# Performance work log

Measured on AMD Instinct MI355X. Metric: run time of the kernel, lower is better.

Reference implementation:

```python
import jax, jax.numpy as jnp
import numpy as np

DIM, N_HEAD, N_KV, HEAD_DIM = 4096, 32, 8, 128
B, S = 2, 2048


def apply_rotary_emb(x, freqs_cis):
    # x: [B, S, H, D]; freqs_cis: [S, D//2, 2]
    xs = x.reshape(x.shape[:-1] + (-1, 2))            # [B,S,H,D/2,2]
    f = freqs_cis.reshape(1, xs.shape[1], 1, xs.shape[3], 2)
    x0, x1 = xs[..., 0], xs[..., 1]
    f0, f1 = f[..., 0], f[..., 1]
    out = jnp.stack([x0 * f0 - x1 * f1, x0 * f1 + x1 * f0], axis=-1)
    return out.reshape(x.shape).astype(x.dtype)


def setup_inputs() -> dict:
    key = jax.random.key(0)
    k1, k2, k3, k4 = jax.random.split(key, 4)
    x = jax.random.normal(k1, (B, S, DIM), dtype=jnp.float32)
    freqs_cis = jax.random.normal(k2, (S, HEAD_DIM // 2, 2), dtype=jnp.float32)
    # causal boolean mask (True = attend)
    mask_cache = jnp.tril(jnp.ones((S, S), dtype=bool))[None, None]
    input_pos = jnp.arange(S, dtype=jnp.int32)
    total_head_dim = (N_HEAD + 2 * N_KV) * HEAD_DIM
    wqkv = jax.random.normal(k3, (total_head_dim, DIM), dtype=jnp.float32) * (DIM ** -0.5)
    wo = jax.random.normal(k4, (DIM, DIM), dtype=jnp.float32) * (DIM ** -0.5)
    return {"x": x, "freqs_cis": freqs_cis, "mask_cache": mask_cache,
            "input_pos": input_pos, "wqkv": wqkv, "wo": wo}


def reference(x, freqs_cis, mask_cache, input_pos, wqkv, wo):
    bsz, seqlen, _ = x.shape
    kv_size = N_KV * HEAD_DIM
    qkv = jnp.einsum('bsd,fd->bsf', x, wqkv)
    q, k, v = jnp.split(qkv, [DIM, DIM + kv_size], axis=-1)
    q = q.reshape(bsz, seqlen, N_HEAD, HEAD_DIM)
    k = k.reshape(bsz, seqlen, N_KV, HEAD_DIM)
    v = v.reshape(bsz, seqlen, N_KV, HEAD_DIM)
    q = apply_rotary_emb(q, freqs_cis)
    k = apply_rotary_emb(k, freqs_cis)
    q = q.transpose(0, 2, 1, 3)   # [B,Hq,S,D]
    k = k.transpose(0, 2, 1, 3)   # [B,Hkv,S,D]
    v = v.transpose(0, 2, 1, 3)
    # GQA: repeat kv heads to match query heads
    g = N_HEAD // N_KV
    k = jnp.repeat(k, g, axis=1)
    v = jnp.repeat(v, g, axis=1)
    scale = 1.0 / jnp.sqrt(jnp.asarray(HEAD_DIM, dtype=q.dtype))
    scores = jnp.einsum('bhqd,bhkd->bhqk', q, k) * scale
    neg_inf = jnp.asarray(jnp.finfo(scores.dtype).min, dtype=scores.dtype)
    scores = jnp.where(mask_cache, scores, neg_inf)
    attn = jax.nn.softmax(scores, axis=-1)
    y = jnp.einsum('bhqk,bhkd->bhqd', attn, v)
    y = y.transpose(0, 2, 1, 3).reshape(bsz, seqlen, DIM)
    return jnp.einsum('bsd,od->bso', y, wo)
```

## Files before the change

### kernel.cpp

```cpp
#include <hip/hip_runtime.h>
#include <hip/hip_bf16.h>

#define DIM   4096
#define NHEAD 32
#define NKV   8
#define HD    128
#define BATCH 2
#define SEQ   2048
#define M1    (BATCH*SEQ)
#define NF    ((NHEAD+2*NKV)*HD)

typedef __attribute__((ext_vector_type(8))) short short8;
typedef __attribute__((ext_vector_type(4))) short short4v;
typedef __attribute__((ext_vector_type(4))) float f32x4;

__device__ __forceinline__ float bf2f(short s) {
    unsigned u = ((unsigned)(unsigned short)s) << 16;
    return __builtin_bit_cast(float, u);
}
__device__ __forceinline__ short f2bf(float f) {
    unsigned u = __builtin_bit_cast(unsigned, f);
    u = u + 0x7fffu + ((u >> 16) & 1u);
    return (short)(u >> 16);
}

__device__ __forceinline__ void gload_lds16(const void* g, void* l) {
    __builtin_amdgcn_global_load_lds(
        (const __attribute__((address_space(1))) void*)g,
        (__attribute__((address_space(3))) void*)l, 16, 0, 0);
}

__global__ void f2bf_k(const float* __restrict__ src, short* __restrict__ dst, int n4) {
    int i = blockIdx.x * blockDim.x + threadIdx.x;
    if (i >= n4) return;
    float4 v = ((const float4*)src)[i];
    short4v o;
    o[0] = f2bf(v.x); o[1] = f2bf(v.y); o[2] = f2bf(v.z); o[3] = f2bf(v.w);
    ((short4v*)dst)[i] = o;
}

template<int OUT_BF16>
__global__ __launch_bounds__(512, 2) void gemm256(const short* __restrict__ A,
                                                  const short* __restrict__ Bm,
                                                  void* __restrict__ Cout,
                                                  int M, int N, int K) {
    __shared__ __align__(16) short As[2][2][128*64];
    __shared__ __align__(16) short Bs[2][2][128*64];
    const int nbn = N >> 8;
    const int nwg = gridDim.x;
    const int cpx = nwg >> 3;
    const int swz = (blockIdx.x & 7) * cpx + (blockIdx.x >> 3);
    const int brow = swz / nbn, bcol = swz % nbn;
    const int t = threadIdx.x, lane = t & 63, w = t >> 6;
    const int wm = w >> 2, wn = w & 3;
    const int l16 = lane & 15, lhi = lane >> 4, l7 = l16 & 7;
    const size_t abase = (size_t)brow * 256 * K;
    const size_t bbase = (size_t)bcol * 256 * K;
    const int sr = t >> 3;
    const int sc = t & 7;
    const int scl = sc ^ (sr & 7);
    f32x4 acc[8][4] = {};

    auto stageA = [&](int kt, int qm) {
#pragma unroll
        for (int i = 0; i < 2; ++i)
            gload_lds16(A + abase + (size_t)(i*128 + qm*64 + sr) * K + kt*64 + scl*8,
                        &As[kt & 1][qm][(i*64 + sr)*64 + sc*8]);
    };
    auto stageB = [&](int kt, int qn) {
#pragma unroll
        for (int i = 0; i < 2; ++i)
            gload_lds16(Bm + bbase + (size_t)((i*2 + (sr>>5))*64 + qn*32 + (sr & 31)) * K + kt*64 + scl*8,
                        &Bs[kt & 1][qn][(i*64 + sr)*64 + sc*8]);
    };

    const int NT = K >> 6;
    stageA(0, 0); stageB(0, 0); stageA(0, 1); stageB(0, 1);
    stageA(1, 0); stageB(1, 0);
    asm volatile("s_waitcnt vmcnt(4)" ::: "memory");
    __builtin_amdgcn_s_barrier();

    short8 a0[4][2], a1[4][2], b0[2][2], b1[2][2];

#define LD_A(dst, P, QM)                                                        \
    _Pragma("unroll") for (int mi = 0; mi < 4; ++mi)                            \
    _Pragma("unroll") for (int kk = 0; kk < 2; ++kk)                            \
        dst[mi][kk] = *(const short8*)&As[P][QM][(wm*64 + mi*16 + l16)*64 + (((kk*4 + lhi) ^ l7) * 8)];
#define LD_B(dst, P, QN)                                                        \
    _Pragma("unroll") for (int ni = 0; ni < 2; ++ni)                            \
    _Pragma("unroll") for (int kk = 0; kk < 2; ++kk)                            \
        dst[ni][kk] = *(const short8*)&Bs[P][QN][(wn*32 + ni*16 + l16)*64 + (((kk*4 + lhi) ^ l7) * 8)];
#define MMA(QM, QN, af, bf)                                                     \
    __builtin_amdgcn_s_barrier();                                               \
    __builtin_amdgcn_s_setprio(1);                                              \
    _Pragma("unroll") for (int kk = 0; kk < 2; ++kk)                            \
    _Pragma("unroll") for (int mi = 0; mi < 4; ++mi)                            \
    _Pragma("unroll") for (int ni = 0; ni < 2; ++ni)                            \
        acc[QM*4 + mi][QN*2 + ni] = __builtin_amdgcn_mfma_f32_16x16x32_bf16(    \
            af[mi][kk], bf[ni][kk], acc[QM*4 + mi][QN*2 + ni], 0, 0, 0);        \
    __builtin_amdgcn_s_setprio(0);                                              \
    __builtin_amdgcn_s_barrier();

    LD_A(a0, 0, 0)
    LD_B(b0, 0, 0)

    for (int cur = 0; cur < NT; ++cur) {
        const int d = cur & 1, dn = d ^ 1;
        LD_B(b1, d, 1)
        if (cur + 1 < NT) stageA(cur + 1, 1);
        MMA(0, 0, a0, b0)
        asm volatile("s_waitcnt vmcnt(2)" ::: "memory");
        LD_A(a1, d, 1)
        if (cur + 1 < NT) stageB(cur + 1, 1);
        MMA(0, 1, a0, b1)
        LD_A(a0, dn, 0)
        if (cur + 2 < NT) stageA(cur + 2, 0);
        MMA(1, 0, a1, b0)
        asm volatile("s_waitcnt vmcnt(2)" ::: "memory");
        LD_B(b0, dn, 0)
        if (cur + 2 < NT) stageB(cur + 2, 0);
        MMA(1, 1, a1, b1)
    }
#undef LD_A
#undef LD_B
#undef MMA

#pragma unroll
    for (int fm = 0; fm < 8; ++fm)
#pragma unroll
        for (int fn = 0; fn < 4; ++fn)
#pragma unroll
            for (int r = 0; r < 4; ++r) {
                size_t row = (size_t)brow*256 + wm*128 + fm*16 + lhi*4 + r;
                size_t col = (size_t)bcol*256 + wn*64 + fn*16 + l16;
                if (OUT_BF16)
                    ((short*)Cout)[row * N + col] = f2bf(acc[fm][fn][r]);
                else
                    ((float*)Cout)[row * N + col] = acc[fm][fn][r];
            }
}

__global__ void rope_split_k(const short* __restrict__ qkv,
                             const float* __restrict__ freqs,
                             short* __restrict__ qb, short* __restrict__ kb,
                             short* __restrict__ vg) {
    int tid  = blockIdx.x * blockDim.x + threadIdx.x;
    int colg = tid % (NF / 8);
    int row  = tid / (NF / 8);
    if (row >= M1) return;
    int b = row >> 11, s = row & 2047;
    int f = colg << 3;
    int h = f >> 7, d = f & 127;
    short8 v = *(const short8*)&qkv[(size_t)row * NF + f];
    if (h < NHEAD + NKV) {
        const float4 fa = *(const float4*)&freqs[(size_t)(s*64 + (d>>1)) * 2];
        const float4 fb = *(const float4*)&freqs[(size_t)(s*64 + (d>>1)) * 2 + 4];
        float fr[8] = {fa.x, fa.y, fa.z, fa.w, fb.x, fb.y, fb.z, fb.w};
        short8 o;
#pragma unroll
        for (int p = 0; p < 4; ++p) {
            float x0 = bf2f(v[2*p]), x1 = bf2f(v[2*p+1]);
            float c = fr[2*p], sn = fr[2*p+1];
            o[2*p]   = f2bf(x0 * c  - x1 * sn);
            o[2*p+1] = f2bf(x0 * sn + x1 * c);
        }
        if (h < NHEAD)
            *(short8*)&qb[((((size_t)b*NHEAD + h)*SEQ + s) << 7) + d] = o;
        else
            *(short8*)&kb[((((size_t)b*NKV + (h - NHEAD))*SEQ + s) << 7) + d] = o;
    } else {
        int kvh = h - NHEAD - NKV;
        size_t base = (((size_t)b*NKV + kvh) << 18) + (size_t)(s >> 5)*4096 + (s & 31);
#pragma unroll
        for (int j = 0; j < 8; ++j)
            vg[base + (size_t)(d + j) * 32] = v[j];
    }
}

__global__ __launch_bounds__(256, 3) void attn_k(const short* __restrict__ qb_,
                                                 const short* __restrict__ kb_,
                                                 const short* __restrict__ vg_,
                                                 short* __restrict__ yb) {
    __shared__ __align__(16) short Ks[2][32*128];
    __shared__ __align__(16) short Vs[2][128*32];
    __shared__ __align__(16) short Pw[4][32*40];
    const int bid = blockIdx.x;
    const int qt = 15 - (bid >> 6);
    const int bh = bid & 63;
    const int b = bh >> 5, h = bh & 31, kv = h >> 2;
    const int t = threadIdx.x, lane = t & 63, w = t >> 6;
    const int l16 = lane & 15, lhi = lane >> 4;
    const short* Qp = qb_ + (((size_t)(b*NHEAD + h)*SEQ + qt*128 + w*32) << 7);
    const short* Kp = kb_ + (((size_t)(b*NKV + kv)*SEQ) << 7);
    const short* Vp = vg_ + (((size_t)(b*NKV + kv)*SEQ) << 7);
    short8 qf[2][4];
#pragma unroll
    for (int qq = 0; qq < 2; ++qq)
#pragma unroll
        for (int kk = 0; kk < 4; ++kk)
            qf[qq][kk] = *(const short8*)&Qp[(qq*16 + l16)*HD + kk*32 + lhi*8];
    f32x4 oacc[2][8] = {};
    float mrow[2] = {-1e30f, -1e30f};
    float lsum[2] = {0.f, 0.f};
    const int NT = (qt + 1) * 4;
    const int qmaxw = qt*128 + w*32 + 31;
    const float sc = 0.08838834764831845f;

    auto stage = [&](int kt, int buf) {
#pragma unroll
        for (int i = 0; i < 2; ++i) {
            int L = i*256 + t;
            int r = L >> 4, s = L & 15;
            int gs = (s & 8) | ((s & 7) ^ (r & 7));
            gload_lds16(Kp + (size_t)kt*4096 + r*128 + gs*8, &Ks[buf][L*8]);
        }
#pragma unroll
        for (int i = 0; i < 2; ++i) {
            int L = i*256 + t;
            int r8 = L >> 3, s3 = L & 7;
            int gs = s3 ^ (r8 & 7);
            gload_lds16(Vp + (size_t)kt*4096 + (r8*8 + gs)*8, &Vs[buf][L*8]);
        }
    };

    stage(0, 0);
    __syncthreads();
    int cur = 0;
    for (int kt = 0; kt < NT; ++kt) {
        if (kt + 1 < NT) stage(kt + 1, cur ^ 1);
        if (kt*32 <= qmaxw) {
            f32x4 sT[2][2] = {};
#pragma unroll
            for (int kk = 0; kk < 4; ++kk) {
                short8 kf[2];
#pragma unroll
                for (int kb2 = 0; kb2 < 2; ++kb2) {
                    int row = kb2*16 + l16;
                    int ch  = kk*4 + lhi;
                    int chs = (ch & 8) | ((ch & 7) ^ (row & 7));
                    kf[kb2] = *(const short8*)&Ks[cur][row*128 + chs*8];
                }
#pragma unroll
                for (int kb2 = 0; kb2 < 2; ++kb2)
#pragma unroll
                    for (int qq = 0; qq < 2; ++qq)
                        sT[kb2][qq] = __builtin_amdgcn_mfma_f32_16x16x32_bf16(kf[kb2], qf[qq][kk], sT[kb2][qq], 0, 0, 0);
            }
#pragma unroll
            for (int qq = 0; qq < 2; ++qq) {
                int qg = qt*128 + w*32 + qq*16 + l16;
                float tmax = -1e30f;
#pragma unroll
                for (int kb2 = 0; kb2 < 2; ++kb2)
#pragma unroll
                    for (int r = 0; r < 4; ++r) {
                        int kg = kt*32 + kb2*16 + lhi*4 + r;
                        float sv = sT[kb2][qq][r] * sc;
                        sv = (kg > qg) ? -1e30f : sv;
                        sT[kb2][qq][r] = sv;
                        tmax = fmaxf(tmax, sv);
                    }
                tmax = fmaxf(tmax, __shfl_xor(tmax, 16, 64));
                tmax = fmaxf(tmax, __shfl_xor(tmax, 32, 64));
                float mn = fmaxf(mrow[qq], tmax);
                float alpha = __expf(mrow[qq] - mn);
                mrow[qq] = mn;
                float rsum = 0.f;
#pragma unroll
                for (int kb2 = 0; kb2 < 2; ++kb2) {
                    short4v pk;
#pragma unroll
                    for (int r = 0; r < 4; ++r) {
                        float p = __expf(sT[kb2][qq][r] - mn);
                        rsum += p;
                        pk[r] = f2bf(p);
                    }
                    *(short4v*)&Pw[w][(qq*16 + l16)*40 + kb2*16 + lhi*4] = pk;
                }
                rsum += __shfl_xor(rsum, 16, 64);
                rsum += __shfl_xor(rsum, 32, 64);
                lsum[qq] = lsum[qq]*alpha + rsum;
                float a4[4];
#pragma unroll
                for (int r = 0; r < 4; ++r)
                    a4[r] = __shfl(alpha, (lane & 48) | (lhi*4 + r), 64);
#pragma unroll
                for (int n = 0; n < 8; ++n)
#pragma unroll
                    for (int r = 0; r < 4; ++r)
                        oacc[qq][n][r] *= a4[r];
            }
            short8 pf[2];
#pragma unroll
            for (int qq = 0; qq < 2; ++qq)
                pf[qq] = *(const short8*)&Pw[w][(qq*16 + l16)*40 + lhi*8];
#pragma unroll
            for (int n = 0; n < 8; ++n) {
                int d   = n*16 + l16;
                int lch = d*4 + lhi;
                int phys = (lch & ~7) | ((lch & 7) ^ ((lch >> 3) & 7));
                short8 vf = *(const short8*)&Vs[cur][phys*8];
#pragma unroll
                for (int qq = 0; qq < 2; ++qq)
                    oacc[qq][n] = __builtin_amdgcn_mfma_f32_16x16x32_bf16(pf[qq], vf, oacc[qq][n], 0, 0, 0);
            }
        }
        __syncthreads();
        cur ^= 1;
    }
#pragma unroll
    for (int qq = 0; qq < 2; ++qq) {
        float inv = 1.f / lsum[qq];
        float i4[4];
#pragma unroll
        for (int r = 0; r < 4; ++r)
            i4[r] = __shfl(inv, (lane & 48) | (lhi*4 + r), 64);
#pragma unroll
        for (int n = 0; n < 8; ++n)
#pragma unroll
            for (int r = 0; r < 4; ++r) {
                size_t row = (size_t)b*SEQ + qt*128 + w*32 + qq*16 + lhi*4 + r;
                yb[row*DIM + h*HD + n*16 + l16] = f2bf(oacc[qq][n][r] * i4[r]);
            }
    }
}

extern "C" void kernel_launch(void* const* d_in, const int* in_sizes, int n_in,
                              void* d_out, int out_size, void* d_ws, size_t ws_size,
                              hipStream_t stream) {
    const float* x     = (const float*)d_in[0];
    const float* freqs = (const float*)d_in[1];
    const float* wqkv  = (const float*)d_in[4];
    const float* wo    = (const float*)d_in[5];
    float* out = (float*)d_out;
    char* ws = (char*)d_ws;
    const size_t MB = 1024*1024;
    short* xb    = (short*)ws;
    short* yb    = (short*)ws;
    short* wqkvb = (short*)(ws + 32*MB);
    short* wob   = (short*)(ws + 32*MB);
    short* qkvb  = (short*)(ws + 80*MB);
    short* qb    = (short*)(ws + 128*MB);
    short* kb    = (short*)(ws + 160*MB);
    short* vg    = (short*)(ws + 168*MB);

    f2bf_k<<<(DIM*DIM/4 + 255)/256, 256, 0, stream>>>(x, xb, DIM*DIM/4);
    f2bf_k<<<(NF*DIM/4 + 255)/256, 256, 0, stream>>>(wqkv, wqkvb, NF*DIM/4);
    gemm256<1><<<(M1/256)*(NF/256), 512, 0, stream>>>(xb, wqkvb, qkvb, M1, NF, DIM);
    rope_split_k<<<(M1*(NF/8) + 255)/256, 256, 0, stream>>>(qkvb, freqs, qb, kb, vg);
    attn_k<<<BATCH*NHEAD*(SEQ/128), 256, 0, stream>>>(qb, kb, vg, yb);
    f2bf_k<<<(DIM*DIM/4 + 255)/256, 256, 0, stream>>>(wo, wob, DIM*DIM/4);
    gemm256<0><<<(M1/256)*(DIM/256), 512, 0, stream>>>(yb, wob, out, M1, DIM, DIM);
}
```

Measured before the change: 554.7 us.

## Restructure GEMM main loop into two-tile unrolled pipeline with full-tile prefetch

Rewrites the GEMM K-loop to process two K-tiles per iteration, with each LDS buffer statically indexed. The prologue now prefetches both halves of the second tile. Global-to-LDS staging is interleaved between MFMA quadrants, and explicit lgkmcnt waits are added. The aim is more overlap of global loads with MFMA work and less per-iteration indexing overhead, at the cost of more complex wait counts and the assumption that NT is even.

```diff
diff --git a/kernel.cpp b/kernel.cpp
--- a/kernel.cpp
+++ b/kernel.cpp
@@ -75,9 +75,10 @@
     };
 
     const int NT = K >> 6;
+    const int NI = NT >> 1;
     stageA(0, 0); stageB(0, 0); stageA(0, 1); stageB(0, 1);
-    stageA(1, 0); stageB(1, 0);
-    asm volatile("s_waitcnt vmcnt(4)" ::: "memory");
+    stageA(1, 0); stageB(1, 0); stageA(1, 1); stageB(1, 1);
+    asm volatile("s_waitcnt vmcnt(6)" ::: "memory");
     __builtin_amdgcn_s_barrier();
 
     short8 a0[4][2], a1[4][2], b0[2][2], b1[2][2];
@@ -100,30 +101,47 @@
             af[mi][kk], bf[ni][kk], acc[QM*4 + mi][QN*2 + ni], 0, 0, 0);        \
     __builtin_amdgcn_s_setprio(0);                                              \
     __builtin_amdgcn_s_barrier();
+#define LGKM8 asm volatile("s_waitcnt lgkmcnt(8)" ::: "memory");
 
     LD_A(a0, 0, 0)
-    LD_B(b0, 0, 0)
-
-    for (int cur = 0; cur < NT; ++cur) {
-        const int d = cur & 1, dn = d ^ 1;
-        LD_B(b1, d, 1)
-        if (cur + 1 < NT) stageA(cur + 1, 1);
+
+    for (int j = 0; j < NI; ++j) {
+        const int v = 2*j + 2;
+        const bool lastI = (j + 1 >= NI);
+        LD_B(b0, 0, 0)
+        if (!lastI) stageA(v, 0);
         MMA(0, 0, a0, b0)
-        asm volatile("s_waitcnt vmcnt(2)" ::: "memory");
-        LD_A(a1, d, 1)
-        if (cur + 1 < NT) stageB(cur + 1, 1);
+        LD_B(b1, 0, 1)
+        LD_A(a1, 0, 1)
+        if (!lastI) stageB(v, 0);
+        LGKM8
         MMA(0, 1, a0, b1)
-        LD_A(a0, dn, 0)
-        if (cur + 2 < NT) stageA(cur + 2, 0);
+        if (!lastI) stageA(v, 1);
         MMA(1, 0, a1, b0)
-        asm volatile("s_waitcnt vmcnt(2)" ::: "memory");
-        LD_B(b0, dn, 0)
-        if (cur + 2 < NT) stageB(cur + 2, 0);
+        if (!lastI) stageB(v, 1);
+        if (lastI) { asm volatile("s_waitcnt vmcnt(0)" ::: "memory"); }
+        else       { asm volatile("s_waitcnt vmcnt(6)" ::: "memory"); }
+        MMA(1, 1, a1, b1)
+        LD_A(a0, 1, 0)
+        LD_B(b0, 1, 0)
+        LGKM8
+        MMA(0, 0, a0, b0)
+        LD_B(b1, 1, 1)
+        LD_A(a1, 1, 1)
+        if (!lastI) { stageA(v + 1, 0); stageB(v + 1, 0); }
+        LGKM8
+        MMA(0, 1, a0, b1)
+        if (!lastI) stageA(v + 1, 1);
+        MMA(1, 0, a1, b0)
+        if (!lastI) LD_A(a0, 0, 0)
+        if (!lastI) stageB(v + 1, 1);
+        if (!lastI) { asm volatile("s_waitcnt vmcnt(6)" ::: "memory"); }
         MMA(1, 1, a1, b1)
     }
 #undef LD_A
 #undef LD_B
 #undef MMA
+#undef LGKM8
 
 #pragma unroll
     for (int fm = 0; fm < 8; ++fm)
```

Measured after the change: 832.4 us. 1.5x slower.
